# Performance work log

Measured on AMD Instinct MI355X. Metric: run time of the kernel, lower is better.

The kernel has to match this reference:

```python
import jax, jax.numpy as jnp
import numpy as np

N_NODES = 50000
N_EDGES = 500000
IN_CH = 128
OUT_CH = 64
HEADS = 4


def setup_inputs() -> dict:
    key = jax.random.key(0)
    ks = jax.random.split(key, 9)
    x = jax.random.normal(ks[0], (N_NODES, IN_CH), dtype=jnp.float32)
    edge_index = jax.random.randint(ks[1], (2, N_EDGES), 0, N_NODES, dtype=jnp.int64)
    edge_weights = jax.random.uniform(ks[2], (N_EDGES, 1), dtype=jnp.float32)
    # xavier-uniform params, stored as [in, out] so y = x @ W
    def xavier(k, shape):
        fan_in, fan_out = shape
        lim = float(np.sqrt(6.0 / (fan_in + fan_out)))
        return jax.random.uniform(k, shape, minval=-lim, maxval=lim, dtype=jnp.float32)
    Wq = xavier(ks[3], (IN_CH, OUT_CH * HEADS))
    Wk = xavier(ks[4], (IN_CH, OUT_CH * HEADS))
    Wv = xavier(ks[5], (IN_CH, OUT_CH * HEADS))
    We = xavier(ks[6], (1, HEADS))
    Wout = xavier(ks[7], (OUT_CH * HEADS, OUT_CH))
    b_out = jnp.zeros((OUT_CH,), dtype=jnp.float32)
    return {"x": x, "edge_index": edge_index, "edge_weights": edge_weights,
            "Wq": Wq, "Wk": Wk, "Wv": Wv, "We": We, "Wout": Wout, "b_out": b_out}


def reference(x, edge_index, edge_weights, Wq, Wk, Wv, We, Wout, b_out):
    num_nodes = x.shape[0]
    src = edge_index[0]
    tgt = edge_index[1]
    x_src = x[src]                                    # [E, in]
    x_tgt = x[tgt]                                    # [E, in]
    q = (x_tgt @ Wq).reshape(-1, HEADS, OUT_CH)       # [E, H, C]
    k = (x_src @ Wk).reshape(-1, HEADS, OUT_CH)
    v = (x_src @ Wv).reshape(-1, HEADS, OUT_CH)
    attn = jnp.sum(q * k, axis=-1) / jnp.sqrt(jnp.float32(OUT_CH))  # [E, H]
    attn = attn + edge_weights @ We                   # [E, H]
    attn = jax.nn.leaky_relu(attn, negative_slope=0.2)
    attn = jax.nn.softmax(attn, axis=0)               # global softmax over edges (as in source)
    weighted_v = attn[..., None] * v                  # [E, H, C]
    out = jax.ops.segment_sum(weighted_v, tgt, num_segments=num_nodes)  # [N, H, C]
    out = out.reshape(num_nodes, HEADS * OUT_CH) @ Wout + b_out         # [N, out]
    if x.shape == out.shape:
        out = out + x
    return out
```

## Files before the change

kernel.cpp:

```cpp
#include <hip/hip_runtime.h>
#include <hip/hip_bf16.h>
#include <hip/hip_fp16.h>

#define N_NODES 50000
#define N_EDGES 500000
#define IN_CH   128
#define D       256
#define UDIM    512
#define OUT_CH  64
#define HEADS   4
#define NC      49
#define PCAP    1024

#define NB_X16  6250
#define NB_HIST 1954
#define NB_MB   256
#define NB_ZB   128
#define NB_GEMM 1564
#define NB_SCAT 1954

typedef _Float16 half8 __attribute__((ext_vector_type(8)));
typedef _Float16 half2_t __attribute__((ext_vector_type(2)));
typedef float   floatx4 __attribute__((ext_vector_type(4)));

__global__ __launch_bounds__(256) void k1_prep_kernel(const float* __restrict__ x,
                                                      __half* __restrict__ x16,
                                                      const int* __restrict__ ei,
                                                      int* __restrict__ cnt,
                                                      double* __restrict__ S,
                                                      const float* __restrict__ Wq,
                                                      const float* __restrict__ Wk,
                                                      const float* __restrict__ Wv,
                                                      const float* __restrict__ Wout,
                                                      __half* __restrict__ M16t,
                                                      __half* __restrict__ Zc16t) {
    __shared__ float sbuf[4][64];
    const int b = blockIdx.x, tid = threadIdx.x;
    if (b < NB_X16) {
        int i = b * 256 + tid;
        if (i < HEADS) S[i] = 0.0;
        int k = i * 4;
        if (k < N_NODES * IN_CH) {
            float4 v = *(const float4*)(x + k);
            union { __half2 h[2]; uint2 u; } pk;
            pk.h[0] = __floats2half2_rn(v.x, v.y);
            pk.h[1] = __floats2half2_rn(v.z, v.w);
            *(uint2*)(x16 + k) = pk.u;
        }
    } else if (b < NB_X16 + NB_HIST) {
        int e = (b - NB_X16) * 256 + tid;
        if (e < N_EDGES) atomicAdd(&cnt[ei[N_EDGES + e]], 1);
    } else if (b < NB_X16 + NB_HIST + NB_MB) {
        const int r = (b - NB_X16 - NB_HIST) * 2 + (tid >> 7);
        const int i = tid & 127;
        const int h = r >> 7, j = r & 127;
        float* buf = sbuf[tid >> 7];
        if (i < 64) buf[i] = Wk[(size_t)j * D + h * 64 + i];
        __syncthreads();
        const float4* qr = (const float4*)(Wq + (size_t)i * D + h * 64);
        float s = 0.f;
        #pragma unroll
        for (int c4 = 0; c4 < 16; ++c4) {
            float4 q = qr[c4];
            s += q.x * buf[c4 * 4] + q.y * buf[c4 * 4 + 1]
               + q.z * buf[c4 * 4 + 2] + q.w * buf[c4 * 4 + 3];
        }
        M16t[(size_t)r * IN_CH + i] = __float2half(s);
    } else {
        const int r = (b - NB_X16 - NB_HIST - NB_MB) * 4 + (tid >> 6);
        const int c = tid & 63;
        const int h = r >> 7, i = r & 127;
        float* buf = sbuf[tid >> 6];
        buf[c] = Wv[(size_t)i * D + h * 64 + c];
        __syncthreads();
        float s = 0.f;
        #pragma unroll 8
        for (int j = 0; j < 64; ++j)
            s += buf[j] * Wout[(size_t)(h * 64 + j) * OUT_CH + c];
        Zc16t[(size_t)c * UDIM + r] = __float2half(s);
    }
}

__global__ __launch_bounds__(256) void k2_scan_reduce_kernel(const int* __restrict__ cnt,
                                                             int* __restrict__ csum) {
    const int b = blockIdx.x, tid = threadIdx.x;
    const int lane = tid & 63, wid = tid >> 6;
    int s = 0;
    int idx0 = b * 1024 + tid * 4;
    #pragma unroll
    for (int i = 0; i < 4; ++i) {
        int idx = idx0 + i;
        if (idx < N_NODES) s += cnt[idx];
    }
    #pragma unroll
    for (int m = 1; m < 64; m <<= 1) s += __shfl_xor(s, m, 64);
    __shared__ int w4[4];
    if (lane == 0) w4[wid] = s;
    __syncthreads();
    if (tid == 0) csum[b] = w4[0] + w4[1] + w4[2] + w4[3];
}

__global__ __launch_bounds__(256) void k3_scan_chunks_kernel(int* __restrict__ cnt,
                                                             const int* __restrict__ csum,
                                                             int* __restrict__ rp) {
    __shared__ int stop[64];
    __shared__ int wsum[4];
    const int b = blockIdx.x, tid = threadIdx.x;
    const int lane = tid & 63, wid = tid >> 6;
    if (tid < 64) stop[tid] = (tid < NC) ? csum[tid] : 0;
    __syncthreads();
    int base = 0;
    for (int w = 0; w < b; ++w) base += stop[w];
    int v[4];
    const int idx0 = b * 1024 + tid * 4;
    #pragma unroll
    for (int i = 0; i < 4; ++i) {
        int idx = idx0 + i;
        v[i] = (idx < N_NODES) ? cnt[idx] : 0;
    }
    int tsum = v[0] + v[1] + v[2] + v[3];
    int x = tsum;
    #pragma unroll
    for (int d = 1; d < 64; d <<= 1) {
        int y = __shfl_up(x, d, 64);
        if (lane >= d) x += y;
    }
    if (lane == 63) wsum[wid] = x;
    __syncthreads();
    int woff = 0;
    for (int w = 0; w < wid; ++w) woff += wsum[w];
    int excl = base + woff + x - tsum;
    #pragma unroll
    for (int i = 0; i < 4; ++i) {
        int idx = idx0 + i;
        if (idx < N_NODES) { rp[idx] = excl; cnt[idx] = excl; }
        excl += v[i];
    }
}

__global__ __launch_bounds__(256) void k4_gemmu_scatter_kernel(const __half* __restrict__ x16,
                                                               const __half* __restrict__ M16t,
                                                               __half* __restrict__ u16,
                                                               const int* __restrict__ ei,
                                                               const float* __restrict__ ew,
                                                               int* __restrict__ cnt,
                                                               int2* __restrict__ payload) {
    __shared__ __half Ax[128][136];
    __shared__ __half Bm[128][136];
    const int tid = threadIdx.x;
    if (blockIdx.x >= NB_GEMM) {
        int e = (blockIdx.x - NB_GEMM) * 256 + tid;
        if (e < N_EDGES) {
            int s = ei[e], t = ei[N_EDGES + e];
            int pos = atomicAdd(&cnt[t], 1);
            payload[pos] = make_int2(s, __float_as_int(ew[e]));
        }
        return;
    }
    const int m0 = (blockIdx.x % 391) * 128;
    const int colbase = (blockIdx.x / 391) * 128;
    {
        const int r = tid >> 1, part = tid & 1;
        uint4 va[8];
        if (m0 + r < N_NODES) {
            const uint4* src = (const uint4*)(x16 + (size_t)(m0 + r) * IN_CH + part * 64);
            #pragma unroll
            for (int q = 0; q < 8; ++q) va[q] = src[q];
        } else {
            #pragma unroll
            for (int q = 0; q < 8; ++q) va[q] = make_uint4(0u, 0u, 0u, 0u);
        }
        uint4* da = (uint4*)&Ax[r][part * 64];
        #pragma unroll
        for (int q = 0; q < 8; ++q) da[q] = va[q];
        const uint4* sb = (const uint4*)(M16t + (size_t)(colbase + r) * IN_CH + part * 64);
        uint4* db = (uint4*)&Bm[r][part * 64];
        #pragma unroll
        for (int q = 0; q < 8; ++q) db[q] = sb[q];
    }
    __syncthreads();

    const int w = tid >> 6, lane = tid & 63;
    const int mrow = lane & 15, quad = lane >> 4;

    half8 a[2][4];
    #pragma unroll
    for (int mt = 0; mt < 2; ++mt)
        #pragma unroll
        for (int ks = 0; ks < 4; ++ks)
            a[mt][ks] = *(const half8*)&Ax[w * 32 + mt * 16 + mrow][ks * 32 + quad * 8];

    floatx4 acc[2][8];
    #pragma unroll
    for (int mt = 0; mt < 2; ++mt)
        #pragma unroll
        for (int nt = 0; nt < 8; ++nt)
            acc[mt][nt] = (floatx4){0.f, 0.f, 0.f, 0.f};

    #pragma unroll
    for (int nt = 0; nt < 8; ++nt) {
        #pragma unroll
        for (int ks = 0; ks < 4; ++ks) {
            half8 bfr = *(const half8*)&Bm[nt * 16 + mrow][ks * 32 + quad * 8];
            acc[0][nt] = __builtin_amdgcn_mfma_f32_16x16x32_f16(a[0][ks], bfr, acc[0][nt], 0, 0, 0);
            acc[1][nt] = __builtin_amdgcn_mfma_f32_16x16x32_f16(a[1][ks], bfr, acc[1][nt], 0, 0, 0);
        }
    }
    __syncthreads();
    #pragma unroll
    for (int mt = 0; mt < 2; ++mt)
        #pragma unroll
        for (int nt = 0; nt < 8; ++nt)
            #pragma unroll
            for (int r = 0; r < 4; ++r)
                Ax[w * 32 + mt * 16 + quad * 4 + r][nt * 16 + mrow] = __float2half(acc[mt][nt][r]);
    __syncthreads();
    {
        const int r = tid >> 1, part = tid & 1;
        if (m0 + r < N_NODES) {
            const uint4* s4 = (const uint4*)&Ax[r][part * 64];
            uint4* d4 = (uint4*)(u16 + (size_t)(m0 + r) * UDIM + colbase + part * 64);
            #pragma unroll
            for (int q = 0; q < 8; ++q) d4[q] = s4[q];
        }
    }
}

__global__ __launch_bounds__(256) void edge_fused_kernel(const __half* __restrict__ u16,
                                                         const __half* __restrict__ x16,
                                                         const int* __restrict__ rp,
                                                         const int* __restrict__ cnt,
                                                         const int2* __restrict__ payload,
                                                         const float* __restrict__ We,
                                                         __half* __restrict__ y16,
                                                         double* __restrict__ S) {
    __shared__ int2 pbuf[PCAP];
    __shared__ float sblk[4];
    const int tid = threadIdx.x;
    const int nodebase = blockIdx.x * 16;

    const int span0 = rp[nodebase];
    const int span1 = cnt[nodebase + 15];
    const int span_len = min(span1 - span0, PCAP);
    for (int i = tid; i < span_len; i += 256) pbuf[i] = payload[span0 + i];
    if (tid < 4) sblk[tid] = 0.f;
    __syncthreads();

    const int l16 = tid & 15;
    const int h = l16 >> 2;
    const int q = l16 & 3;
    const int node = nodebase + (tid >> 4);
    const float wev = We[h];

    uint4 ur4[4];
    {
        const uint4* ub = (const uint4*)(u16 + (size_t)node * UDIM + h * 128 + q * 32);
        ur4[0] = ub[0]; ur4[1] = ub[1]; ur4[2] = ub[2]; ur4[3] = ub[3];
    }
    const half2_t* uh = (const half2_t*)ur4;

    half2_t yacc[16];
    #pragma unroll
    for (int t = 0; t < 16; ++t) yacc[t] = (half2_t){(_Float16)0.f, (_Float16)0.f};

    float sacc = 0.f;
    const int start = rp[node];
    const int end = cnt[node];

    auto getpl = [&](int e) -> int2 {
        int idx = e - span0;
        return (idx < PCAP) ? pbuf[idx] : payload[e];
    };

    int2 pl = make_int2(0, 0);
    uint4 xr[4];
    if (start < end) {
        pl = getpl(start);
        const uint4* xb = (const uint4*)(x16 + (size_t)pl.x * IN_CH + q * 32);
        xr[0] = xb[0]; xr[1] = xb[1]; xr[2] = xb[2]; xr[3] = xb[3];
    }
    for (int e = start; e < end; ++e) {
        int2 pln = pl;
        uint4 xrn[4] = {xr[0], xr[1], xr[2], xr[3]};
        if (e + 1 < end) {
            pln = getpl(e + 1);
            const uint4* xb = (const uint4*)(x16 + (size_t)pln.x * IN_CH + q * 32);
            xrn[0] = xb[0]; xrn[1] = xb[1]; xrn[2] = xb[2]; xrn[3] = xb[3];
        }
        const half2_t* xh = (const half2_t*)xr;
        float dot = 0.f;
        #pragma unroll
        for (int t = 0; t < 16; ++t)
            dot = __builtin_amdgcn_fdot2(uh[t], xh[t], dot, false);
        dot += __shfl_xor(dot, 1, 16);
        dot += __shfl_xor(dot, 2, 16);
        float l = dot * 0.125f + __int_as_float(pl.y) * wev;
        l = fmaxf(l, 0.2f * l);
        float p = __expf(l);
        if (q == 0) sacc += p;
        half2_t p2 = (half2_t){(_Float16)p, (_Float16)p};
        #pragma unroll
        for (int t = 0; t < 16; ++t)
            yacc[t] = p2 * xh[t] + yacc[t];
        pl = pln;
        xr[0] = xrn[0]; xr[1] = xrn[1]; xr[2] = xrn[2]; xr[3] = xrn[3];
    }
    {
        uint4* yo = (uint4*)(y16 + (size_t)node * UDIM + h * 128 + q * 32);
        const uint4* ys = (const uint4*)yacc;
        yo[0] = ys[0]; yo[1] = ys[1]; yo[2] = ys[2]; yo[3] = ys[3];
    }
    __syncthreads();
    if (q == 0) atomicAdd(&sblk[h], sacc);
    __syncthreads();
    if (tid < 4) atomicAdd(&S[tid], (double)sblk[tid]);
}

__global__ __launch_bounds__(256) void gemm_out_mfma_kernel(const __half* __restrict__ y16,
                                                            const __half* __restrict__ Zc16t,
                                                            const double* __restrict__ S,
                                                            const float* __restrict__ b_out,
                                                            float* __restrict__ out) {
    __shared__ __half Ay[128][136];
    __shared__ __half Bz[64][136];
    __shared__ float invs_s[4];
    const int m0 = blockIdx.x * 128;
    const int tid = threadIdx.x;
    if (tid < 4) invs_s[tid] = (float)(1.0 / S[tid]);

    const int w = tid >> 6, lane = tid & 63;
    const int mrow = lane & 15, quad = lane >> 4;

    floatx4 result[2][4];
    #pragma unroll
    for (int mt = 0; mt < 2; ++mt)
        #pragma unroll
        for (int nt = 0; nt < 4; ++nt)
            result[mt][nt] = (floatx4){0.f, 0.f, 0.f, 0.f};

    for (int h = 0; h < HEADS; ++h) {
        {
            const int r = tid >> 1, part = tid & 1;
            uint4 va[8];
            if (m0 + r < N_NODES) {
                const uint4* src = (const uint4*)(y16 + (size_t)(m0 + r) * UDIM + h * 128 + part * 64);
                #pragma unroll
                for (int qq = 0; qq < 8; ++qq) va[qq] = src[qq];
            } else {
                #pragma unroll
                for (int qq = 0; qq < 8; ++qq) va[qq] = make_uint4(0u, 0u, 0u, 0u);
            }
            uint4* da = (uint4*)&Ay[r][part * 64];
            #pragma unroll
            for (int qq = 0; qq < 8; ++qq) da[qq] = va[qq];
        }
        {
            const int r = tid >> 2, part = tid & 3;
            const uint4* sb = (const uint4*)(Zc16t + (size_t)r * UDIM + h * 128 + part * 32);
            uint4* db = (uint4*)&Bz[r][part * 32];
            #pragma unroll
            for (int qq = 0; qq < 4; ++qq) db[qq] = sb[qq];
        }
        __syncthreads();

        half8 a[2][4];
        #pragma unroll
        for (int mt = 0; mt < 2; ++mt)
            #pragma unroll
            for (int ks = 0; ks < 4; ++ks)
                a[mt][ks] = *(const half8*)&Ay[w * 32 + mt * 16 + mrow][ks * 32 + quad * 8];

        floatx4 acc[2][4];
        #pragma unroll
        for (int mt = 0; mt < 2; ++mt)
            #pragma unroll
            for (int nt = 0; nt < 4; ++nt)
                acc[mt][nt] = (floatx4){0.f, 0.f, 0.f, 0.f};

        #pragma unroll
        for (int nt = 0; nt < 4; ++nt) {
            #pragma unroll
            for (int ks = 0; ks < 4; ++ks) {
                half8 bfr = *(const half8*)&Bz[nt * 16 + mrow][ks * 32 + quad * 8];
                acc[0][nt] = __builtin_amdgcn_mfma_f32_16x16x32_f16(a[0][ks], bfr, acc[0][nt], 0, 0, 0);
                acc[1][nt] = __builtin_amdgcn_mfma_f32_16x16x32_f16(a[1][ks], bfr, acc[1][nt], 0, 0, 0);
            }
        }
        const float inv = invs_s[h];
        #pragma unroll
        for (int mt = 0; mt < 2; ++mt)
            #pragma unroll
            for (int nt = 0; nt < 4; ++nt) {
                result[mt][nt][0] += inv * acc[mt][nt][0];
                result[mt][nt][1] += inv * acc[mt][nt][1];
                result[mt][nt][2] += inv * acc[mt][nt][2];
                result[mt][nt][3] += inv * acc[mt][nt][3];
            }
        __syncthreads();
    }
    float bcol[4];
    #pragma unroll
    for (int nt = 0; nt < 4; ++nt) bcol[nt] = b_out[nt * 16 + mrow];
    #pragma unroll
    for (int mt = 0; mt < 2; ++mt) {
        #pragma unroll
        for (int r = 0; r < 4; ++r) {
            int row = m0 + w * 32 + mt * 16 + quad * 4 + r;
            if (row < N_NODES) {
                float* dst = out + (size_t)row * OUT_CH;
                #pragma unroll
                for (int nt = 0; nt < 4; ++nt)
                    dst[nt * 16 + mrow] = result[mt][nt][r] + bcol[nt];
            }
        }
    }
}

extern "C" void kernel_launch(void* const* d_in, const int* in_sizes, int n_in,
                              void* d_out, int out_size, void* d_ws, size_t ws_size,
                              hipStream_t stream) {
    const float* x     = (const float*)d_in[0];
    const int*   ei    = (const int*)d_in[1];
    const float* ew    = (const float*)d_in[2];
    const float* Wq    = (const float*)d_in[3];
    const float* Wk    = (const float*)d_in[4];
    const float* Wv    = (const float*)d_in[5];
    const float* We    = (const float*)d_in[6];
    const float* Wout  = (const float*)d_in[7];
    const float* b_out = (const float*)d_in[8];
    float* out = (float*)d_out;

    __half* u16   = (__half*)d_ws;
    __half* y16   = u16 + (size_t)N_NODES * UDIM;
    __half* x16   = y16 + (size_t)N_NODES * UDIM;
    double* S     = (double*)(x16 + (size_t)N_NODES * IN_CH);
    __half* M16t  = (__half*)(S + HEADS);
    __half* Zc16t = M16t + UDIM * IN_CH;
    int*    rp    = (int*)(Zc16t + OUT_CH * UDIM);
    int*    cnt   = rp + N_NODES;
    int*    csum  = cnt + N_NODES;
    int2*   payload = (int2*)(csum + 64);

    hipMemsetAsync(cnt, 0, N_NODES * sizeof(int), stream);
    k1_prep_kernel<<<NB_X16 + NB_HIST + NB_MB + NB_ZB, 256, 0, stream>>>(
        x, x16, ei, cnt, S, Wq, Wk, Wv, Wout, M16t, Zc16t);
    k2_scan_reduce_kernel<<<NC, 256, 0, stream>>>(cnt, csum);
    k3_scan_chunks_kernel<<<NC, 256, 0, stream>>>(cnt, csum, rp);
    k4_gemmu_scatter_kernel<<<NB_GEMM + NB_SCAT, 256, 0, stream>>>(
        x16, M16t, u16, ei, ew, cnt, payload);
    edge_fused_kernel<<<N_NODES / 16, 256, 0, stream>>>(u16, x16, rp, cnt, payload, We, y16, S);
    gemm_out_mfma_kernel<<<(N_NODES + 127) / 128, 256, 0, stream>>>(y16, Zc16t, S, b_out, out);
}
```

Baseline: 270.5 us.

## Fuse per-node U projection GEMM into edge aggregation kernel via LDS

The U = x·M projection is now computed per 32-node tile inside the edge aggregation kernel and kept in LDS, so the 50000x512 fp16 u16 buffer is never written to or read back from global memory. Each block handles a tile and a pair of heads, with the edge scatter moved into its own small kernel. The cross-lane dot reduction switches from shuffles to DPP moves and uses four independent fdot2 chains. In exchange, the GEMM B operand is read straight from global memory without LDS staging, the per-span payload LDS cache shrinks, and the payload/x gathers are now done twice (once per head-pair block).

Measured after the change: 319.6 us. 18.2% more time.

```diff
diff --git a/kernel.cpp b/kernel.cpp
--- a/kernel.cpp
+++ b/kernel.cpp
@@ -10,18 +10,26 @@
 #define OUT_CH  64
 #define HEADS   4
 #define NC      49
-#define PCAP    1024
 
 #define NB_X16  6250
 #define NB_HIST 1954
 #define NB_MB   256
 #define NB_ZB   128
-#define NB_GEMM 1564
 #define NB_SCAT 1954
+#define NPB     32
+#define NTILE   1563
+#define PCAP    512
 
 typedef _Float16 half8 __attribute__((ext_vector_type(8)));
 typedef _Float16 half2_t __attribute__((ext_vector_type(2)));
 typedef float   floatx4 __attribute__((ext_vector_type(4)));
+
+__device__ __forceinline__ float dpp_xor1(float x) {
+    return __int_as_float(__builtin_amdgcn_mov_dpp(__float_as_int(x), 0xB1, 0xf, 0xf, true));
+}
+__device__ __forceinline__ float dpp_xor2(float x) {
+    return __int_as_float(__builtin_amdgcn_mov_dpp(__float_as_int(x), 0x4E, 0xf, 0xf, true));
+}
 
 __global__ __launch_bounds__(256) void k1_prep_kernel(const float* __restrict__ x,
                                                       __half* __restrict__ x16,
@@ -138,182 +146,155 @@
     }
 }
 
-__global__ __launch_bounds__(256) void k4_gemmu_scatter_kernel(const __half* __restrict__ x16,
-                                                               const __half* __restrict__ M16t,
-                                                               __half* __restrict__ u16,
-                                                               const int* __restrict__ ei,
-                                                               const float* __restrict__ ew,
-                                                               int* __restrict__ cnt,
-                                                               int2* __restrict__ payload) {
-    __shared__ __half Ax[128][136];
-    __shared__ __half Bm[128][136];
+__global__ __launch_bounds__(256) void k4b_scatter_kernel(const int* __restrict__ ei,
+                                                          const float* __restrict__ ew,
+                                                          int* __restrict__ cnt,
+                                                          int2* __restrict__ payload) {
+    int e = blockIdx.x * 256 + threadIdx.x;
+    if (e < N_EDGES) {
+        int s = ei[e], t = ei[N_EDGES + e];
+        int pos = atomicAdd(&cnt[t], 1);
+        payload[pos] = make_int2(s, __float_as_int(ew[e]));
+    }
+}
+
+__global__ __launch_bounds__(256) void fused_ue_kernel(const __half* __restrict__ x16,
+                                                       const __half* __restrict__ M16t,
+                                                       const int* __restrict__ rp,
+                                                       const int* __restrict__ cnt,
+                                                       const int2* __restrict__ payload,
+                                                       const float* __restrict__ We,
+                                                       __half* __restrict__ y16,
+                                                       double* __restrict__ S) {
+    __shared__ __half u_lds[NPB][264];
+    __shared__ int2 pbuf[PCAP];
+    __shared__ float sblk[2];
     const int tid = threadIdx.x;
-    if (blockIdx.x >= NB_GEMM) {
-        int e = (blockIdx.x - NB_GEMM) * 256 + tid;
-        if (e < N_EDGES) {
-            int s = ei[e], t = ei[N_EDGES + e];
-            int pos = atomicAdd(&cnt[t], 1);
-            payload[pos] = make_int2(s, __float_as_int(ew[e]));
-        }
-        return;
-    }
-    const int m0 = (blockIdx.x % 391) * 128;
-    const int colbase = (blockIdx.x / 391) * 128;
-    {
-        const int r = tid >> 1, part = tid & 1;
-        uint4 va[8];
-        if (m0 + r < N_NODES) {
-            const uint4* src = (const uint4*)(x16 + (size_t)(m0 + r) * IN_CH + part * 64);
-            #pragma unroll
-            for (int q = 0; q < 8; ++q) va[q] = src[q];
-        } else {
-            #pragma unroll
-            for (int q = 0; q < 8; ++q) va[q] = make_uint4(0u, 0u, 0u, 0u);
-        }
-        uint4* da = (uint4*)&Ax[r][part * 64];
-        #pragma unroll
-        for (int q = 0; q < 8; ++q) da[q] = va[q];
-        const uint4* sb = (const uint4*)(M16t + (size_t)(colbase + r) * IN_CH + part * 64);
-        uint4* db = (uint4*)&Bm[r][part * 64];
-        #pragma unroll
-        for (int q = 0; q < 8; ++q) db[q] = sb[q];
-    }
-    __syncthreads();
+    const int tile = blockIdx.x >> 1;
+    const int hp = blockIdx.x & 1;
+    const int nb0 = tile * NPB;
+    const int nlast = min(nb0 + NPB - 1, N_NODES - 1);
+
+    const int span0 = rp[nb0];
+    const int span1 = cnt[nlast];
+    const int span_len = min(span1 - span0, PCAP);
+    for (int i = tid; i < span_len; i += 256) pbuf[i] = payload[span0 + i];
+    if (tid < 2) sblk[tid] = 0.f;
 
     const int w = tid >> 6, lane = tid & 63;
     const int mrow = lane & 15, quad = lane >> 4;
 
     half8 a[2][4];
     #pragma unroll
+    for (int mt = 0; mt < 2; ++mt) {
+        int row = min(nb0 + mt * 16 + mrow, N_NODES - 1);
+        const __half* ab = x16 + (size_t)row * IN_CH + quad * 8;
+        #pragma unroll
+        for (int ks = 0; ks < 4; ++ks) a[mt][ks] = *(const half8*)(ab + ks * 32);
+    }
+
+    floatx4 acc[2][4];
+    #pragma unroll
     for (int mt = 0; mt < 2; ++mt)
         #pragma unroll
-        for (int ks = 0; ks < 4; ++ks)
-            a[mt][ks] = *(const half8*)&Ax[w * 32 + mt * 16 + mrow][ks * 32 + quad * 8];
-
-    floatx4 acc[2][8];
-    #pragma unroll
-    for (int mt = 0; mt < 2; ++mt)
-        #pragma unroll
-        for (int nt = 0; nt < 8; ++nt)
+        for (int nt = 0; nt < 4; ++nt)
             acc[mt][nt] = (floatx4){0.f, 0.f, 0.f, 0.f};
 
     #pragma unroll
-    for (int nt = 0; nt < 8; ++nt) {
+    for (int nt = 0; nt < 4; ++nt) {
+        const __half* bb = M16t + (size_t)(hp * 256 + w * 64 + nt * 16 + mrow) * IN_CH + quad * 8;
         #pragma unroll
         for (int ks = 0; ks < 4; ++ks) {
-            half8 bfr = *(const half8*)&Bm[nt * 16 + mrow][ks * 32 + quad * 8];
+            half8 bfr = *(const half8*)(bb + ks * 32);
             acc[0][nt] = __builtin_amdgcn_mfma_f32_16x16x32_f16(a[0][ks], bfr, acc[0][nt], 0, 0, 0);
             acc[1][nt] = __builtin_amdgcn_mfma_f32_16x16x32_f16(a[1][ks], bfr, acc[1][nt], 0, 0, 0);
         }
     }
+    #pragma unroll
+    for (int mt = 0; mt < 2; ++mt)
+        #pragma unroll
+        for (int nt = 0; nt < 4; ++nt)
+            #pragma unroll
+            for (int r = 0; r < 4; ++r)
+                u_lds[mt * 16 + quad * 4 + r][w * 64 + nt * 16 + mrow] = __float2half(acc[mt][nt][r]);
     __syncthreads();
-    #pragma unroll
-    for (int mt = 0; mt < 2; ++mt)
-        #pragma unroll
-        for (int nt = 0; nt < 8; ++nt)
-            #pragma unroll
-            for (int r = 0; r < 4; ++r)
-                Ax[w * 32 + mt * 16 + quad * 4 + r][nt * 16 + mrow] = __float2half(acc[mt][nt][r]);
+
+    const int g = tid >> 3;
+    const int l8 = tid & 7;
+    const int hq = l8 >> 2;
+    const int q = l8 & 3;
+    const int node = nb0 + g;
+    const int h = hp * 2 + hq;
+    const float wev = We[h];
+
+    if (node < N_NODES) {
+        uint4 ur4[4];
+        {
+            const uint4* ub = (const uint4*)&u_lds[g][hq * 128 + q * 32];
+            ur4[0] = ub[0]; ur4[1] = ub[1]; ur4[2] = ub[2]; ur4[3] = ub[3];
+        }
+        const half2_t* uh = (const half2_t*)ur4;
+
+        half2_t yacc[16];
+        #pragma unroll
+        for (int t = 0; t < 16; ++t) yacc[t] = (half2_t){(_Float16)0.f, (_Float16)0.f};
+
+        float sacc = 0.f;
+        const int start = rp[node];
+        const int end = cnt[node];
+
+        auto getpl = [&](int e) -> int2 {
+            int idx = e - span0;
+            return (idx < PCAP) ? pbuf[idx] : payload[e];
+        };
+
+        int2 pl = make_int2(0, 0);
+        uint4 xr[4];
+        if (start < end) {
+            pl = getpl(start);
+            const uint4* xb = (const uint4*)(x16 + (size_t)pl.x * IN_CH + q * 32);
+            xr[0] = xb[0]; xr[1] = xb[1]; xr[2] = xb[2]; xr[3] = xb[3];
+        }
+        for (int e = start; e < end; ++e) {
+            int2 pln = pl;
+            uint4 xrn[4] = {xr[0], xr[1], xr[2], xr[3]};
+            if (e + 1 < end) {
+                pln = getpl(e + 1);
+                const uint4* xb = (const uint4*)(x16 + (size_t)pln.x * IN_CH + q * 32);
+                xrn[0] = xb[0]; xrn[1] = xb[1]; xrn[2] = xb[2]; xrn[3] = xb[3];
+            }
+            const half2_t* xh = (const half2_t*)xr;
+            float d0 = 0.f, d1 = 0.f, d2 = 0.f, d3 = 0.f;
+            #pragma unroll
+            for (int t = 0; t < 4; ++t) {
+                d0 = __builtin_amdgcn_fdot2(uh[t],      xh[t],      d0, false);
+                d1 = __builtin_amdgcn_fdot2(uh[t + 4],  xh[t + 4],  d1, false);
+                d2 = __builtin_amdgcn_fdot2(uh[t + 8],  xh[t + 8],  d2, false);
+                d3 = __builtin_amdgcn_fdot2(uh[t + 12], xh[t + 12], d3, false);
+            }
+            float dot = (d0 + d1) + (d2 + d3);
+            dot += dpp_xor1(dot);
+            dot += dpp_xor2(dot);
+            float l = dot * 0.125f + __int_as_float(pl.y) * wev;
+            l = fmaxf(l, 0.2f * l);
+            float p = __expf(l);
+            sacc += (q == 0) ? p : 0.f;
+            half2_t p2 = (half2_t){(_Float16)p, (_Float16)p};
+            #pragma unroll
+            for (int t = 0; t < 16; ++t)
+                yacc[t] = p2 * xh[t] + yacc[t];
+            pl = pln;
+            xr[0] = xrn[0]; xr[1] = xrn[1]; xr[2] = xrn[2]; xr[3] = xrn[3];
+        }
+        {
+            uint4* yo = (uint4*)(y16 + (size_t)node * UDIM + h * 128 + q * 32);
+            const uint4* ys = (const uint4*)yacc;
+            yo[0] = ys[0]; yo[1] = ys[1]; yo[2] = ys[2]; yo[3] = ys[3];
+        }
+        if (q == 0) atomicAdd(&sblk[hq], sacc);
+    }
     __syncthreads();
-    {
-        const int r = tid >> 1, part = tid & 1;
-        if (m0 + r < N_NODES) {
-            const uint4* s4 = (const uint4*)&Ax[r][part * 64];
-            uint4* d4 = (uint4*)(u16 + (size_t)(m0 + r) * UDIM + colbase + part * 64);
-            #pragma unroll
-            for (int q = 0; q < 8; ++q) d4[q] = s4[q];
-        }
-    }
-}
-
-__global__ __launch_bounds__(256) void edge_fused_kernel(const __half* __restrict__ u16,
-                                                         const __half* __restrict__ x16,
-                                                         const int* __restrict__ rp,
-                                                         const int* __restrict__ cnt,
-                                                         const int2* __restrict__ payload,
-                                                         const float* __restrict__ We,
-                                                         __half* __restrict__ y16,
-                                                         double* __restrict__ S) {
-    __shared__ int2 pbuf[PCAP];
-    __shared__ float sblk[4];
-    const int tid = threadIdx.x;
-    const int nodebase = blockIdx.x * 16;
-
-    const int span0 = rp[nodebase];
-    const int span1 = cnt[nodebase + 15];
-    const int span_len = min(span1 - span0, PCAP);
-    for (int i = tid; i < span_len; i += 256) pbuf[i] = payload[span0 + i];
-    if (tid < 4) sblk[tid] = 0.f;
-    __syncthreads();
-
-    const int l16 = tid & 15;
-    const int h = l16 >> 2;
-    const int q = l16 & 3;
-    const int node = nodebase + (tid >> 4);
-    const float wev = We[h];
-
-    uint4 ur4[4];
-    {
-        const uint4* ub = (const uint4*)(u16 + (size_t)node * UDIM + h * 128 + q * 32);
-        ur4[0] = ub[0]; ur4[1] = ub[1]; ur4[2] = ub[2]; ur4[3] = ub[3];
-    }
-    const half2_t* uh = (const half2_t*)ur4;
-
-    half2_t yacc[16];
-    #pragma unroll
-    for (int t = 0; t < 16; ++t) yacc[t] = (half2_t){(_Float16)0.f, (_Float16)0.f};
-
-    float sacc = 0.f;
-    const int start = rp[node];
-    const int end = cnt[node];
-
-    auto getpl = [&](int e) -> int2 {
-        int idx = e - span0;
-        return (idx < PCAP) ? pbuf[idx] : payload[e];
-    };
-
-    int2 pl = make_int2(0, 0);
-    uint4 xr[4];
-    if (start < end) {
-        pl = getpl(start);
-        const uint4* xb = (const uint4*)(x16 + (size_t)pl.x * IN_CH + q * 32);
-        xr[0] = xb[0]; xr[1] = xb[1]; xr[2] = xb[2]; xr[3] = xb[3];
-    }
-    for (int e = start; e < end; ++e) {
-        int2 pln = pl;
-        uint4 xrn[4] = {xr[0], xr[1], xr[2], xr[3]};
-        if (e + 1 < end) {
-            pln = getpl(e + 1);
-            const uint4* xb = (const uint4*)(x16 + (size_t)pln.x * IN_CH + q * 32);
-            xrn[0] = xb[0]; xrn[1] = xb[1]; xrn[2] = xb[2]; xrn[3] = xb[3];
-        }
-        const half2_t* xh = (const half2_t*)xr;
-        float dot = 0.f;
-        #pragma unroll
-        for (int t = 0; t < 16; ++t)
-            dot = __builtin_amdgcn_fdot2(uh[t], xh[t], dot, false);
-        dot += __shfl_xor(dot, 1, 16);
-        dot += __shfl_xor(dot, 2, 16);
-        float l = dot * 0.125f + __int_as_float(pl.y) * wev;
-        l = fmaxf(l, 0.2f * l);
-        float p = __expf(l);
-        if (q == 0) sacc += p;
-        half2_t p2 = (half2_t){(_Float16)p, (_Float16)p};
-        #pragma unroll
-        for (int t = 0; t < 16; ++t)
-            yacc[t] = p2 * xh[t] + yacc[t];
-        pl = pln;
-        xr[0] = xrn[0]; xr[1] = xrn[1]; xr[2] = xrn[2]; xr[3] = xrn[3];
-    }
-    {
-        uint4* yo = (uint4*)(y16 + (size_t)node * UDIM + h * 128 + q * 32);
-        const uint4* ys = (const uint4*)yacc;
-        yo[0] = ys[0]; yo[1] = ys[1]; yo[2] = ys[2]; yo[3] = ys[3];
-    }
-    __syncthreads();
-    if (q == 0) atomicAdd(&sblk[h], sacc);
-    __syncthreads();
-    if (tid < 4) atomicAdd(&S[tid], (double)sblk[tid]);
+    if (tid < 2) atomicAdd(&S[hp * 2 + tid], (double)sblk[tid]);
 }
 
 __global__ __launch_bounds__(256) void gemm_out_mfma_kernel(const __half* __restrict__ y16,
@@ -446,8 +427,7 @@
         x, x16, ei, cnt, S, Wq, Wk, Wv, Wout, M16t, Zc16t);
     k2_scan_reduce_kernel<<<NC, 256, 0, stream>>>(cnt, csum);
     k3_scan_chunks_kernel<<<NC, 256, 0, stream>>>(cnt, csum, rp);
-    k4_gemmu_scatter_kernel<<<NB_GEMM + NB_SCAT, 256, 0, stream>>>(
-        x16, M16t, u16, ei, ew, cnt, payload);
-    edge_fused_kernel<<<N_NODES / 16, 256, 0, stream>>>(u16, x16, rp, cnt, payload, We, y16, S);
+    k4b_scatter_kernel<<<NB_SCAT, 256, 0, stream>>>(ei, ew, cnt, payload);
+    fused_ue_kernel<<<NTILE * 2, 256, 0, stream>>>(x16, M16t, rp, cnt, payload, We, y16, S);
     gemm_out_mfma_kernel<<<(N_NODES + 127) / 128, 256, 0, stream>>>(y16, Zc16t, S, b_out, out);
 }
```
